# Performance work log

Measured on AMD Instinct MI355X. Metric: run time of the kernel, lower is better.

## Reference

```python
import jax, jax.numpy as jnp
from jax import lax
import numpy as np

H = 256

def _cell(x, h, c, wih, whh, bih, bhh):
    # PyTorch LSTMCell: gates ordered i, f, g, o
    g = x @ wih.T + bih + h @ whh.T + bhh
    i, f, gg, o = jnp.split(g, 4, axis=-1)
    c = jax.nn.sigmoid(f) * c + jax.nn.sigmoid(i) * jnp.tanh(gg)
    h = jax.nn.sigmoid(o) * jnp.tanh(c)
    return h, c


def setup_inputs() -> dict:
    key = jax.random.key(0)
    ks = iter(jax.random.split(key, 64))
    def lin(out_f, in_f):
        s = 1.0 / np.sqrt(in_f)
        w = jax.random.uniform(next(ks), (out_f, in_f), minval=-s, maxval=s, dtype=jnp.float32)
        b = jax.random.uniform(next(ks), (out_f,), minval=-s, maxval=s, dtype=jnp.float32)
        return w, b
    def cellp():
        s = 1.0 / np.sqrt(H)
        return tuple(jax.random.uniform(next(ks), sh, minval=-s, maxval=s, dtype=jnp.float32)
                     for sh in [(4 * H, H), (4 * H, H), (4 * H,), (4 * H,)])
    d = {}
    d['x'] = jax.random.normal(next(ks), (20, 256, 64, 64), dtype=jnp.float32)
    d['fc_en1_w'], d['fc_en1_b'] = lin(1024, 4096)
    d['fc_en2_w'], d['fc_en2_b'] = lin(H, 1024)
    for nm in ['en1', 'en2', 'en3', 'de1', 'de2', 'de3']:
        d[nm + '_wih'], d[nm + '_whh'], d[nm + '_bih'], d[nm + '_bhh'] = cellp()
    d['fc_de1_w'], d['fc_de1_b'] = lin(1024, H)
    d['fc_de2_w'], d['fc_de2_b'] = lin(4096, 1024)
    d['future_step'] = 10
    return d


def reference(x, fc_en1_w, fc_en1_b, fc_en2_w, fc_en2_b,
              en1_wih, en1_whh, en1_bih, en1_bhh,
              en2_wih, en2_whh, en2_bih, en2_bhh,
              en3_wih, en3_whh, en3_bih, en3_bhh,
              de1_wih, de1_whh, de1_bih, de1_bhh,
              de2_wih, de2_whh, de2_bih, de2_bhh,
              de3_wih, de3_whh, de3_bih, de3_bhh,
              fc_de1_w, fc_de1_b, fc_de2_w, fc_de2_b, future_step):
    seq, B = x.shape[0], x.shape[1]
    xf = x.reshape(seq, B, -1)  # (S, B, 4096)
    z0 = jnp.zeros((B, H), x.dtype)

    def enc_step(carry, xt):
        h1, c1, h2, c2, h3, c3 = carry
        z = jax.nn.relu(xt @ fc_en1_w.T + fc_en1_b)
        z = jax.nn.relu(z @ fc_en2_w.T + fc_en2_b)
        h1, c1 = _cell(z, h1, c1, en1_wih, en1_whh, en1_bih, en1_bhh)
        h2, c2 = _cell(h1, h2, c2, en2_wih, en2_whh, en2_bih, en2_bhh)
        h3, c3 = _cell(h2, h3, c3, en3_wih, en3_whh, en3_bih, en3_bhh)
        return (h1, c1, h2, c2, h3, c3), None

    enc_carry, _ = lax.scan(enc_step, (z0,) * 6, xf)
    h_e3 = enc_carry[4]

    def dec_step(carry, _):
        h1, c1, h2, c2, h3, c3 = carry
        h1, c1 = _cell(z0, h1, c1, de1_wih, de1_whh, de1_bih, de1_bhh)
        h2, c2 = _cell(h1, h2, c2, de2_wih, de2_whh, de2_bih, de2_bhh)
        h3, c3 = _cell(h2, h3, c3, de3_wih, de3_whh, de3_bih, de3_bhh)
        y = jax.nn.relu(h3 @ fc_de1_w.T + fc_de1_b)
        y = jnp.tanh(y @ fc_de2_w.T + fc_de2_b)
        return (h1, c1, h2, c2, h3, c3), y

    _, ys = lax.scan(dec_step, (h_e3, z0, z0, z0, z0, z0), None, length=future_step)
    return ys.reshape(future_step, B, 64, 64)
```

## Files before the change

kernel.cpp:

```cpp
#include <hip/hip_runtime.h>
#include <math.h>

static __device__ __forceinline__ float sigf(float v) { return 1.0f / (1.0f + expf(-v)); }

using s8v  = __attribute__((ext_vector_type(8))) short;
using f4v  = __attribute__((ext_vector_type(4))) float;

static __device__ __forceinline__ void splitf(float f, unsigned short& h, unsigned short& l) {
  unsigned u = __float_as_uint(f);
  unsigned short hb = (unsigned short)((u + 0x7FFFu + ((u >> 16) & 1u)) >> 16);
  float hf = __uint_as_float(((unsigned)hb) << 16);
  float lf = f - hf;
  unsigned ul = __float_as_uint(lf);
  unsigned short lb = (unsigned short)((ul + 0x7FFFu + ((ul >> 16) & 1u)) >> 16);
  h = hb; l = lb;
}

__global__ __launch_bounds__(256) void gemm_mfma(
    const float* __restrict__ A, const float* __restrict__ W,
    const float* __restrict__ bias, float* __restrict__ C,
    int M, int N, int K, int act)
{
  __shared__ unsigned short AsH[128 * 40];
  __shared__ unsigned short AsL[128 * 40];
  __shared__ unsigned short WsH[64 * 40];
  __shared__ unsigned short WsL[64 * 40];

  const int t = threadIdx.x;
  const int w = t >> 6, lane = t & 63;
  const int lrow = lane & 15, lk = (lane >> 4) * 8;
  const int m0 = blockIdx.x * 128, n0 = blockIdx.y * 64;

  f4v acc[2][4];
#pragma unroll
  for (int i = 0; i < 2; ++i)
#pragma unroll
    for (int j = 0; j < 4; ++j) acc[i][j] = (f4v){0.f, 0.f, 0.f, 0.f};

  for (int k0 = 0; k0 < K; k0 += 32) {
#pragma unroll
    for (int i = 0; i < 4; ++i) {
      int v = i * 256 + t;
      int row = v >> 3, kq = (v & 7) << 2;
      float4 a = *(const float4*)(A + (size_t)(m0 + row) * K + k0 + kq);
      ushort4 h4, l4;
      splitf(a.x, h4.x, l4.x); splitf(a.y, h4.y, l4.y);
      splitf(a.z, h4.z, l4.z); splitf(a.w, h4.w, l4.w);
      *(ushort4*)&AsH[row * 40 + kq] = h4;
      *(ushort4*)&AsL[row * 40 + kq] = l4;
    }
#pragma unroll
    for (int i = 0; i < 2; ++i) {
      int v = i * 256 + t;
      int row = v >> 3, kq = (v & 7) << 2;
      float4 b = *(const float4*)(W + (size_t)(n0 + row) * K + k0 + kq);
      ushort4 h4, l4;
      splitf(b.x, h4.x, l4.x); splitf(b.y, h4.y, l4.y);
      splitf(b.z, h4.z, l4.z); splitf(b.w, h4.w, l4.w);
      *(ushort4*)&WsH[row * 40 + kq] = h4;
      *(ushort4*)&WsL[row * 40 + kq] = l4;
    }
    __syncthreads();

    s8v aH[2], aL[2], bH[4], bL[4];
#pragma unroll
    for (int mt = 0; mt < 2; ++mt) {
      int r = (w * 32 + mt * 16 + lrow) * 40 + lk;
      aH[mt] = *(const s8v*)&AsH[r];
      aL[mt] = *(const s8v*)&AsL[r];
    }
#pragma unroll
    for (int nt = 0; nt < 4; ++nt) {
      int r = (nt * 16 + lrow) * 40 + lk;
      bH[nt] = *(const s8v*)&WsH[r];
      bL[nt] = *(const s8v*)&WsL[r];
    }

#pragma unroll
    for (int mt = 0; mt < 2; ++mt)
#pragma unroll
      for (int nt = 0; nt < 4; ++nt) {
        acc[mt][nt] = __builtin_amdgcn_mfma_f32_16x16x32_bf16(aH[mt], bH[nt], acc[mt][nt], 0, 0, 0);
        acc[mt][nt] = __builtin_amdgcn_mfma_f32_16x16x32_bf16(aH[mt], bL[nt], acc[mt][nt], 0, 0, 0);
        acc[mt][nt] = __builtin_amdgcn_mfma_f32_16x16x32_bf16(aL[mt], bH[nt], acc[mt][nt], 0, 0, 0);
      }
    __syncthreads();
  }

#pragma unroll
  for (int mt = 0; mt < 2; ++mt)
#pragma unroll
    for (int nt = 0; nt < 4; ++nt) {
      int gcol = n0 + nt * 16 + lrow;
      float bv = bias[gcol];
#pragma unroll
      for (int r = 0; r < 4; ++r) {
        int grow = m0 + w * 32 + mt * 16 + (lane >> 4) * 4 + r;
        float v = acc[mt][nt][r] + bv;
        if (act == 1) v = fmaxf(v, 0.f);
        else if (act == 2) v = tanhf(v);
        C[(size_t)grow * N + gcol] = v;
      }
    }
}

__global__ __launch_bounds__(256) void gemm64(
    const float* __restrict__ A, const float* __restrict__ Bw,
    const float* __restrict__ bias, float* __restrict__ C,
    int M, int N, int K, int act)
{
  __shared__ float As[16][68];
  __shared__ float Bs[16][68];
  const int tid = threadIdx.x;
  const int tm = tid & 15, tn = tid >> 4;
  const int m0 = blockIdx.x * 64, n0 = blockIdx.y * 64;
  float acc[4][4];
#pragma unroll
  for (int i = 0; i < 4; ++i)
#pragma unroll
    for (int j = 0; j < 4; ++j) acc[i][j] = 0.f;

  for (int k0 = 0; k0 < K; k0 += 16) {
    {
      int row = tid >> 2, kc = (tid & 3) << 2;
      float4 a = *(const float4*)(A + (size_t)(m0 + row) * K + k0 + kc);
      As[kc + 0][row] = a.x; As[kc + 1][row] = a.y;
      As[kc + 2][row] = a.z; As[kc + 3][row] = a.w;
      float4 b = *(const float4*)(Bw + (size_t)(n0 + row) * K + k0 + kc);
      Bs[kc + 0][row] = b.x; Bs[kc + 1][row] = b.y;
      Bs[kc + 2][row] = b.z; Bs[kc + 3][row] = b.w;
    }
    __syncthreads();
#pragma unroll
    for (int k = 0; k < 16; ++k) {
      float av[4], bv[4];
      *(float4*)(av) = *(const float4*)&As[k][tm * 4];
      *(float4*)(bv) = *(const float4*)&Bs[k][tn * 4];
#pragma unroll
      for (int i = 0; i < 4; ++i)
#pragma unroll
        for (int j = 0; j < 4; ++j) acc[i][j] = fmaf(av[i], bv[j], acc[i][j]);
    }
    __syncthreads();
  }
#pragma unroll
  for (int i = 0; i < 4; ++i) {
    int row = m0 + tm * 4 + i;
    float o[4];
#pragma unroll
    for (int j = 0; j < 4; ++j) {
      float v = acc[i][j] + bias[n0 + tn * 4 + j];
      if (act == 1) v = fmaxf(v, 0.f);
      else if (act == 2) v = tanhf(v);
      o[j] = v;
    }
    *(float4*)(C + (size_t)row * N + n0 + tn * 4) = *(float4*)o;
  }
}

__global__ __launch_bounds__(256) void prep_pack(
    const float* __restrict__ wih, const float* __restrict__ whh,
    const float* __restrict__ bih, const float* __restrict__ bhh,
    float* __restrict__ wihP, float* __restrict__ whhP, float* __restrict__ bP)
{
  const int j = blockIdx.x, k = threadIdx.x;
  float4 a, c;
  a.x = wih[(0 * 256 + j) * 256 + k];
  a.y = wih[(1 * 256 + j) * 256 + k];
  a.z = wih[(2 * 256 + j) * 256 + k];
  a.w = wih[(3 * 256 + j) * 256 + k];
  *(float4*)&wihP[((size_t)j * 256 + k) * 4] = a;
  c.x = whh[(0 * 256 + j) * 256 + k];
  c.y = whh[(1 * 256 + j) * 256 + k];
  c.z = whh[(2 * 256 + j) * 256 + k];
  c.w = whh[(3 * 256 + j) * 256 + k];
  *(float4*)&whhP[((size_t)j * 256 + k) * 4] = c;
  if (k < 4) bP[j * 4 + k] = bih[k * 256 + j] + bhh[k * 256 + j];
}

__global__ __launch_bounds__(256) void transpose256(
    const float* __restrict__ in, float* __restrict__ out)
{
  const int t = blockIdx.x, c4 = blockIdx.y;
  const int r = threadIdx.x;
  float4 v = *(const float4*)(in + ((size_t)t * 256 + r) * 256 + c4 * 4);
  float* op = out + (size_t)t * 65536 + (size_t)(c4 * 4) * 256 + r;
  op[0]   = v.x;
  op[256] = v.y;
  op[512] = v.z;
  op[768] = v.w;
}

struct CellSlot {
  const float* x;
  const float* wih;
  const float* whh;
  const float* bias;
  const float* hin;
  float* c;
  float* hout;
  float* hcopy;
  int hasx;
};
struct CellArgs { CellSlot s[3]; };

__global__ __launch_bounds__(256) void cell_multi(CellArgs args)
{
  const CellSlot S = args.s[blockIdx.x >> 8];
  const int inner = blockIdx.x & 255;
  const int jg = inner & 63, bg = inner >> 6;
  const int t = threadIdx.x;
  const int lane = t & 63;
  const int b = bg * 64 + lane;

  const int jw = __builtin_amdgcn_readfirstlane(jg * 4 + (t >> 6));
  const float4* wh = (const float4*)(S.whh + (size_t)jw * 1024);
  const float4* wi = (const float4*)(S.wih + (size_t)jw * 1024);
  const float* hcol = S.hin + b;
  float4 acc = *(const float4*)(S.bias + jw * 4);

  if (S.hasx) {
    const float* xcol = S.x + b;
#pragma unroll 8
    for (int k = 0; k < 256; ++k) {
      const float hv = hcol[k * 256];
      const float4 wv = wh[k];
      acc.x = fmaf(hv, wv.x, acc.x);
      acc.y = fmaf(hv, wv.y, acc.y);
      acc.z = fmaf(hv, wv.z, acc.z);
      acc.w = fmaf(hv, wv.w, acc.w);
      const float xv = xcol[k * 256];
      const float4 vv = wi[k];
      acc.x = fmaf(xv, vv.x, acc.x);
      acc.y = fmaf(xv, vv.y, acc.y);
      acc.z = fmaf(xv, vv.z, acc.z);
      acc.w = fmaf(xv, vv.w, acc.w);
    }
  } else {
#pragma unroll 8
    for (int k = 0; k < 256; ++k) {
      const float hv = hcol[k * 256];
      const float4 wv = wh[k];
      acc.x = fmaf(hv, wv.x, acc.x);
      acc.y = fmaf(hv, wv.y, acc.y);
      acc.z = fmaf(hv, wv.z, acc.z);
      acc.w = fmaf(hv, wv.w, acc.w);
    }
  }

  const int idx = jw * 256 + b;
  const float cold = S.c[idx];
  const float ig = sigf(acc.x), fg = sigf(acc.y);
  const float gg = tanhf(acc.z), og = sigf(acc.w);
  const float cn = fg * cold + ig * gg;
  const float hn = og * tanhf(cn);
  S.c[idx] = cn;
  S.hout[idx] = hn;
  if (S.hcopy) S.hcopy[idx] = hn;
}


extern "C" void kernel_launch(void* const* d_in, const int* in_sizes, int n_in,
                              void* d_out, int out_size, void* d_ws, size_t ws_size,
                              hipStream_t stream)
{
  const float* x_in  = (const float*)d_in[0];
  const float* w_en1 = (const float*)d_in[1];
  const float* b_en1 = (const float*)d_in[2];
  const float* w_en2 = (const float*)d_in[3];
  const float* b_en2 = (const float*)d_in[4];
  const float* cw[6][4];
  for (int i = 0; i < 6; ++i)
    for (int j = 0; j < 4; ++j) cw[i][j] = (const float*)d_in[5 + i * 4 + j];
  const float* w_de1 = (const float*)d_in[29];
  const float* b_de1 = (const float*)d_in[30];
  const float* w_de2 = (const float*)d_in[31];
  const float* b_de2 = (const float*)d_in[32];
  float* out = (float*)d_out;

  float* ws   = (float*)d_ws;
  float* wihP = ws;
  float* whhP = wihP + 6 * 262144;
  float* bP   = whhP + 6 * 262144;
  float* hb   = bP + 6 * 1024;
  float* cb   = hb + 12 * 65536;
  float* H3T  = cb + 6 * 65536;
  float* R1   = H3T + 10 * 65536;
  float* R2   = R1 + 5242880;

  for (int i = 0; i < 6; ++i)
    prep_pack<<<256, 256, 0, stream>>>(cw[i][0], cw[i][1], cw[i][2], cw[i][3],
                                       wihP + i * 262144, whhP + i * 262144,
                                       bP + i * 1024);
  hipMemsetAsync(hb, 0, (size_t)18 * 65536 * sizeof(float), stream);

  float* z1  = R1;
  float* z2  = R2;
  float* z2T = R1;
  gemm_mfma<<<dim3(5120 / 128, 1024 / 64), 256, 0, stream>>>(
      x_in, w_en1, b_en1, z1, 5120, 1024, 4096, 1);
  gemm64<<<dim3(5120 / 64, 256 / 64), 256, 0, stream>>>(
      z1, w_en2, b_en2, z2, 5120, 256, 1024, 1);
  transpose256<<<dim3(20, 64), 256, 0, stream>>>(z2, z2T);

  int pp[6] = {0, 0, 0, 0, 0, 0};
  auto HBuf = [&](int l, int p) { return hb + (size_t)(l * 2 + p) * 65536; };
  auto CBuf = [&](int l) { return cb + (size_t)l * 65536; };
  auto WI = [&](int l) { return wihP + (size_t)l * 262144; };
  auto WH = [&](int l) { return whhP + (size_t)l * 262144; };
  auto BB = [&](int l) { return bP + (size_t)l * 1024; };

  for (int s = 0; s <= 21; ++s) {
    CellArgs a; int n = 0; int tog[3]; int nt = 0;
    if (s < 20) {
      a.s[n++] = {z2T + (size_t)s * 65536, WI(0), WH(0), BB(0),
                  HBuf(0, pp[0]), CBuf(0), HBuf(0, pp[0] ^ 1), nullptr, 1};
      tog[nt++] = 0;
    }
    if (s >= 1 && s <= 20) {
      a.s[n++] = {HBuf(0, pp[0]), WI(1), WH(1), BB(1),
                  HBuf(1, pp[1]), CBuf(1), HBuf(1, pp[1] ^ 1), nullptr, 1};
      tog[nt++] = 1;
    }
    if (s >= 2) {
      a.s[n++] = {HBuf(1, pp[1]), WI(2), WH(2), BB(2),
                  HBuf(2, pp[2]), CBuf(2), HBuf(2, pp[2] ^ 1), nullptr, 1};
      tog[nt++] = 2;
    }
    cell_multi<<<n * 256, 256, 0, stream>>>(a);
    for (int i = 0; i < nt; ++i) pp[tog[i]] ^= 1;
  }

  for (int s = 0; s <= 11; ++s) {
    CellArgs a; int n = 0; int tog[3]; int nt = 0;
    if (s < 10) {
      const float* h1in = (s == 0) ? HBuf(2, pp[2]) : HBuf(3, pp[3]);
      a.s[n++] = {nullptr, WI(3), WH(3), BB(3),
                  h1in, CBuf(3), HBuf(3, pp[3] ^ 1), nullptr, 0};
      tog[nt++] = 3;
    }
    if (s >= 1 && s <= 10) {
      a.s[n++] = {HBuf(3, pp[3]), WI(4), WH(4), BB(4),
                  HBuf(4, pp[4]), CBuf(4), HBuf(4, pp[4] ^ 1), nullptr, 1};
      tog[nt++] = 4;
    }
    if (s >= 2) {
      a.s[n++] = {HBuf(4, pp[4]), WI(5), WH(5), BB(5),
                  HBuf(5, pp[5]), CBuf(5), HBuf(5, pp[5] ^ 1),
                  H3T + (size_t)(s - 2) * 65536, 1};
      tog[nt++] = 5;
    }
    cell_multi<<<n * 256, 256, 0, stream>>>(a);
    for (int i = 0; i < nt; ++i) pp[tog[i]] ^= 1;
  }

  float* H3std = R1;
  float* y1    = R1 + 1310720;
  transpose256<<<dim3(10, 64), 256, 0, stream>>>(H3T, H3std);
  gemm64<<<dim3(2560 / 64, 1024 / 64), 256, 0, stream>>>(
      H3std, w_de1, b_de1, y1, 2560, 1024, 256, 1);
  gemm_mfma<<<dim3(2560 / 128, 4096 / 64), 256, 0, stream>>>(
      y1, w_de2, b_de2, out, 2560, 4096, 1024, 2);

  (void)in_sizes; (void)n_in; (void)out_size; (void)ws_size;
}
```

Measured before the change: 1.024 ms.

## Pre-split weights and activations to bf16 hi/lo once, use split-bf16 MFMA everywhere

Adds a wsplit kernel that converts each FC weight into bf16 high and low halves once per call, so the GEMM tiles load pre-split bf16 data instead of splitting fp32 per tile. The GEMM epilogues can now write their outputs already split, so the next GEMM (the new gemm_bb) reads bf16 hi/lo pairs directly. The fp32 SIMT gemm64 used for the small FC layers is replaced with the MFMA kernel. This cuts redundant split arithmetic and global traffic, at the cost of extra conversion kernels and workspace.

```diff
diff --git a/kernel.cpp b/kernel.cpp
--- a/kernel.cpp
+++ b/kernel.cpp
@@ -3,8 +3,8 @@
 
 static __device__ __forceinline__ float sigf(float v) { return 1.0f / (1.0f + expf(-v)); }
 
-using s8v  = __attribute__((ext_vector_type(8))) short;
-using f4v  = __attribute__((ext_vector_type(4))) float;
+using s8v = __attribute__((ext_vector_type(8))) short;
+using f4v = __attribute__((ext_vector_type(4))) float;
 
 static __device__ __forceinline__ void splitf(float f, unsigned short& h, unsigned short& l) {
   unsigned u = __float_as_uint(f);
@@ -16,9 +16,27 @@
   h = hb; l = lb;
 }
 
-__global__ __launch_bounds__(256) void gemm_mfma(
-    const float* __restrict__ A, const float* __restrict__ W,
+__global__ __launch_bounds__(256) void wsplit(
+    const float* __restrict__ W, unsigned short* __restrict__ WH,
+    unsigned short* __restrict__ WL, int n4)
+{
+  int i = blockIdx.x * 256 + threadIdx.x;
+  if (i < n4) {
+    float4 v = ((const float4*)W)[i];
+    ushort4 h, l;
+    splitf(v.x, h.x, l.x); splitf(v.y, h.y, l.y);
+    splitf(v.z, h.z, l.z); splitf(v.w, h.w, l.w);
+    ((ushort4*)WH)[i] = h;
+    ((ushort4*)WL)[i] = l;
+  }
+}
+
+template <int OSPLIT>
+__global__ __launch_bounds__(256) void gemm_sf(
+    const float* __restrict__ A,
+    const unsigned short* __restrict__ WH, const unsigned short* __restrict__ WL,
     const float* __restrict__ bias, float* __restrict__ C,
+    unsigned short* __restrict__ OH, unsigned short* __restrict__ OL,
     int M, int N, int K, int act)
 {
   __shared__ unsigned short AsH[128 * 40];
@@ -49,16 +67,10 @@
       *(ushort4*)&AsH[row * 40 + kq] = h4;
       *(ushort4*)&AsL[row * 40 + kq] = l4;
     }
-#pragma unroll
-    for (int i = 0; i < 2; ++i) {
-      int v = i * 256 + t;
-      int row = v >> 3, kq = (v & 7) << 2;
-      float4 b = *(const float4*)(W + (size_t)(n0 + row) * K + k0 + kq);
-      ushort4 h4, l4;
-      splitf(b.x, h4.x, l4.x); splitf(b.y, h4.y, l4.y);
-      splitf(b.z, h4.z, l4.z); splitf(b.w, h4.w, l4.w);
-      *(ushort4*)&WsH[row * 40 + kq] = h4;
-      *(ushort4*)&WsL[row * 40 + kq] = l4;
+    {
+      int row = t >> 2, q = (t & 3) * 8;
+      *(s8v*)&WsH[row * 40 + q] = *(const s8v*)(WH + (size_t)(n0 + row) * K + k0 + q);
+      *(s8v*)&WsL[row * 40 + q] = *(const s8v*)(WL + (size_t)(n0 + row) * K + k0 + q);
     }
     __syncthreads();
 
@@ -75,7 +87,6 @@
       bH[nt] = *(const s8v*)&WsH[r];
       bL[nt] = *(const s8v*)&WsL[r];
     }
-
 #pragma unroll
     for (int mt = 0; mt < 2; ++mt)
 #pragma unroll
@@ -99,63 +110,103 @@
         float v = acc[mt][nt][r] + bv;
         if (act == 1) v = fmaxf(v, 0.f);
         else if (act == 2) v = tanhf(v);
-        C[(size_t)grow * N + gcol] = v;
+        if (OSPLIT) {
+          unsigned short h, l;
+          splitf(v, h, l);
+          OH[(size_t)grow * N + gcol] = h;
+          OL[(size_t)grow * N + gcol] = l;
+        } else {
+          C[(size_t)grow * N + gcol] = v;
+        }
       }
     }
 }
 
-__global__ __launch_bounds__(256) void gemm64(
-    const float* __restrict__ A, const float* __restrict__ Bw,
+template <int OSPLIT>
+__global__ __launch_bounds__(256) void gemm_bb(
+    const unsigned short* __restrict__ AH, const unsigned short* __restrict__ AL,
+    const unsigned short* __restrict__ WH, const unsigned short* __restrict__ WL,
     const float* __restrict__ bias, float* __restrict__ C,
+    unsigned short* __restrict__ OH, unsigned short* __restrict__ OL,
     int M, int N, int K, int act)
 {
-  __shared__ float As[16][68];
-  __shared__ float Bs[16][68];
-  const int tid = threadIdx.x;
-  const int tm = tid & 15, tn = tid >> 4;
-  const int m0 = blockIdx.x * 64, n0 = blockIdx.y * 64;
-  float acc[4][4];
-#pragma unroll
-  for (int i = 0; i < 4; ++i)
-#pragma unroll
-    for (int j = 0; j < 4; ++j) acc[i][j] = 0.f;
-
-  for (int k0 = 0; k0 < K; k0 += 16) {
+  __shared__ unsigned short AsH[128 * 40];
+  __shared__ unsigned short AsL[128 * 40];
+  __shared__ unsigned short WsH[64 * 40];
+  __shared__ unsigned short WsL[64 * 40];
+
+  const int t = threadIdx.x;
+  const int w = t >> 6, lane = t & 63;
+  const int lrow = lane & 15, lk = (lane >> 4) * 8;
+  const int m0 = blockIdx.x * 128, n0 = blockIdx.y * 64;
+
+  f4v acc[2][4];
+#pragma unroll
+  for (int i = 0; i < 2; ++i)
+#pragma unroll
+    for (int j = 0; j < 4; ++j) acc[i][j] = (f4v){0.f, 0.f, 0.f, 0.f};
+
+  for (int k0 = 0; k0 < K; k0 += 32) {
+#pragma unroll
+    for (int i = 0; i < 2; ++i) {
+      int v = i * 256 + t;
+      int row = v >> 2, q = (v & 3) * 8;
+      *(s8v*)&AsH[row * 40 + q] = *(const s8v*)(AH + (size_t)(m0 + row) * K + k0 + q);
+      *(s8v*)&AsL[row * 40 + q] = *(const s8v*)(AL + (size_t)(m0 + row) * K + k0 + q);
+    }
     {
-      int row = tid >> 2, kc = (tid & 3) << 2;
-      float4 a = *(const float4*)(A + (size_t)(m0 + row) * K + k0 + kc);
-      As[kc + 0][row] = a.x; As[kc + 1][row] = a.y;
-      As[kc + 2][row] = a.z; As[kc + 3][row] = a.w;
-      float4 b = *(const float4*)(Bw + (size_t)(n0 + row) * K + k0 + kc);
-      Bs[kc + 0][row] = b.x; Bs[kc + 1][row] = b.y;
-      Bs[kc + 2][row] = b.z; Bs[kc + 3][row] = b.w;
+      int row = t >> 2, q = (t & 3) * 8;
+      *(s8v*)&WsH[row * 40 + q] = *(const s8v*)(WH + (size_t)(n0 + row) * K + k0 + q);
+      *(s8v*)&WsL[row * 40 + q] = *(const s8v*)(WL + (size_t)(n0 + row) * K + k0 + q);
     }
     __syncthreads();
-#pragma unroll
-    for (int k = 0; k < 16; ++k) {
-      float av[4], bv[4];
-      *(float4*)(av) = *(const float4*)&As[k][tm * 4];
-      *(float4*)(bv) = *(const float4*)&Bs[k][tn * 4];
-#pragma unroll
-      for (int i = 0; i < 4; ++i)
-#pragma unroll
-        for (int j = 0; j < 4; ++j) acc[i][j] = fmaf(av[i], bv[j], acc[i][j]);
-    }
+
+    s8v aH[2], aL[2], bH[4], bL[4];
+#pragma unroll
+    for (int mt = 0; mt < 2; ++mt) {
+      int r = (w * 32 + mt * 16 + lrow) * 40 + lk;
+      aH[mt] = *(const s8v*)&AsH[r];
+      aL[mt] = *(const s8v*)&AsL[r];
+    }
+#pragma unroll
+    for (int nt = 0; nt < 4; ++nt) {
+      int r = (nt * 16 + lrow) * 40 + lk;
+      bH[nt] = *(const s8v*)&WsH[r];
+      bL[nt] = *(const s8v*)&WsL[r];
+    }
+#pragma unroll
+    for (int mt = 0; mt < 2; ++mt)
+#pragma unroll
+      for (int nt = 0; nt < 4; ++nt) {
+        acc[mt][nt] = __builtin_amdgcn_mfma_f32_16x16x32_bf16(aH[mt], bH[nt], acc[mt][nt], 0, 0, 0);
+        acc[mt][nt] = __builtin_amdgcn_mfma_f32_16x16x32_bf16(aH[mt], bL[nt], acc[mt][nt], 0, 0, 0);
+        acc[mt][nt] = __builtin_amdgcn_mfma_f32_16x16x32_bf16(aL[mt], bH[nt], acc[mt][nt], 0, 0, 0);
+      }
     __syncthreads();
   }
-#pragma unroll
-  for (int i = 0; i < 4; ++i) {
-    int row = m0 + tm * 4 + i;
-    float o[4];
-#pragma unroll
-    for (int j = 0; j < 4; ++j) {
-      float v = acc[i][j] + bias[n0 + tn * 4 + j];
-      if (act == 1) v = fmaxf(v, 0.f);
-      else if (act == 2) v = tanhf(v);
-      o[j] = v;
-    }
-    *(float4*)(C + (size_t)row * N + n0 + tn * 4) = *(float4*)o;
-  }
+
+#pragma unroll
+  for (int mt = 0; mt < 2; ++mt)
+#pragma unroll
+    for (int nt = 0; nt < 4; ++nt) {
+      int gcol = n0 + nt * 16 + lrow;
+      float bv = bias[gcol];
+#pragma unroll
+      for (int r = 0; r < 4; ++r) {
+        int grow = m0 + w * 32 + mt * 16 + (lane >> 4) * 4 + r;
+        float v = acc[mt][nt][r] + bv;
+        if (act == 1) v = fmaxf(v, 0.f);
+        else if (act == 2) v = tanhf(v);
+        if (OSPLIT) {
+          unsigned short h, l;
+          splitf(v, h, l);
+          OH[(size_t)grow * N + gcol] = h;
+          OL[(size_t)grow * N + gcol] = l;
+        } else {
+          C[(size_t)grow * N + gcol] = v;
+        }
+      }
+    }
 }
 
 __global__ __launch_bounds__(256) void prep_pack(
@@ -189,6 +240,21 @@
   op[256] = v.y;
   op[512] = v.z;
   op[768] = v.w;
+}
+
+__global__ __launch_bounds__(256) void transpose256s(
+    const float* __restrict__ in, unsigned short* __restrict__ outH,
+    unsigned short* __restrict__ outL)
+{
+  const int t = blockIdx.x, c4 = blockIdx.y;
+  const int r = threadIdx.x;
+  float4 v = *(const float4*)(in + ((size_t)t * 256 + r) * 256 + c4 * 4);
+  ushort4 h, l;
+  splitf(v.x, h.x, l.x); splitf(v.y, h.y, l.y);
+  splitf(v.z, h.z, l.z); splitf(v.w, h.w, l.w);
+  size_t o = (size_t)t * 65536 + (size_t)(c4 * 4) * 256 + r;
+  outH[o] = h.x; outH[o + 256] = h.y; outH[o + 512] = h.z; outH[o + 768] = h.w;
+  outL[o] = l.x; outL[o + 256] = l.y; outL[o + 512] = l.z; outL[o + 768] = l.w;
 }
 
 struct CellSlot {
@@ -285,22 +351,38 @@
   float* hb   = bP + 6 * 1024;
   float* cb   = hb + 12 * 65536;
   float* H3T  = cb + 6 * 65536;
-  float* R1   = H3T + 10 * 65536;
-  float* R2   = R1 + 5242880;
+  float* z2   = H3T + 10 * 65536;
+  float* z2T  = z2 + 1310720;
+  unsigned short* us = (unsigned short*)(z2T + 1310720);
+  unsigned short* WEN1H = us;              us += 4194304;
+  unsigned short* WEN1L = us;              us += 4194304;
+  unsigned short* WEN2H = us;              us += 262144;
+  unsigned short* WEN2L = us;              us += 262144;
+  unsigned short* WDE1H = us;              us += 262144;
+  unsigned short* WDE1L = us;              us += 262144;
+  unsigned short* WDE2H = us;              us += 4194304;
+  unsigned short* WDE2L = us;              us += 4194304;
+  unsigned short* Z1H   = us;              us += 5242880;
+  unsigned short* Z1L   = us;              us += 5242880;
+  unsigned short* H3H = Z1H;
+  unsigned short* H3L = Z1H + 655360;
+  unsigned short* Y1H = Z1H + 1310720;
+  unsigned short* Y1L = Z1H + 1310720 + 2621440;
 
   for (int i = 0; i < 6; ++i)
     prep_pack<<<256, 256, 0, stream>>>(cw[i][0], cw[i][1], cw[i][2], cw[i][3],
                                        wihP + i * 262144, whhP + i * 262144,
                                        bP + i * 1024);
+  wsplit<<<4096, 256, 0, stream>>>(w_en1, WEN1H, WEN1L, 1048576);
+  wsplit<<<256, 256, 0, stream>>>(w_en2, WEN2H, WEN2L, 65536);
+  wsplit<<<256, 256, 0, stream>>>(w_de1, WDE1H, WDE1L, 65536);
+  wsplit<<<4096, 256, 0, stream>>>(w_de2, WDE2H, WDE2L, 1048576);
   hipMemsetAsync(hb, 0, (size_t)18 * 65536 * sizeof(float), stream);
 
-  float* z1  = R1;
-  float* z2  = R2;
-  float* z2T = R1;
-  gemm_mfma<<<dim3(5120 / 128, 1024 / 64), 256, 0, stream>>>(
-      x_in, w_en1, b_en1, z1, 5120, 1024, 4096, 1);
-  gemm64<<<dim3(5120 / 64, 256 / 64), 256, 0, stream>>>(
-      z1, w_en2, b_en2, z2, 5120, 256, 1024, 1);
+  gemm_sf<1><<<dim3(5120 / 128, 1024 / 64), 256, 0, stream>>>(
+      x_in, WEN1H, WEN1L, b_en1, nullptr, Z1H, Z1L, 5120, 1024, 4096, 1);
+  gemm_bb<0><<<dim3(5120 / 128, 256 / 64), 256, 0, stream>>>(
+      Z1H, Z1L, WEN2H, WEN2L, b_en2, z2, nullptr, nullptr, 5120, 256, 1024, 1);
   transpose256<<<dim3(20, 64), 256, 0, stream>>>(z2, z2T);
 
   int pp[6] = {0, 0, 0, 0, 0, 0};
@@ -354,13 +436,11 @@
     for (int i = 0; i < nt; ++i) pp[tog[i]] ^= 1;
   }
 
-  float* H3std = R1;
-  float* y1    = R1 + 1310720;
-  transpose256<<<dim3(10, 64), 256, 0, stream>>>(H3T, H3std);
-  gemm64<<<dim3(2560 / 64, 1024 / 64), 256, 0, stream>>>(
-      H3std, w_de1, b_de1, y1, 2560, 1024, 256, 1);
-  gemm_mfma<<<dim3(2560 / 128, 4096 / 64), 256, 0, stream>>>(
-      y1, w_de2, b_de2, out, 2560, 4096, 1024, 2);
+  transpose256s<<<dim3(10, 64), 256, 0, stream>>>(H3T, H3H, H3L);
+  gemm_bb<1><<<dim3(2560 / 128, 1024 / 64), 256, 0, stream>>>(
+      H3H, H3L, WDE1H, WDE1L, b_de1, nullptr, Y1H, Y1L, 2560, 1024, 256, 1);
+  gemm_bb<0><<<dim3(2560 / 128, 4096 / 64), 256, 0, stream>>>(
+      Y1H, Y1L, WDE2H, WDE2L, b_de2, out, nullptr, nullptr, 2560, 4096, 1024, 2);
 
   (void)in_sizes; (void)n_in; (void)out_size; (void)ws_size;
 }
```

Result: faster. 945.5 us (-7.7%).
